# Optimization experiments

Measured on AMD Instinct MI355X. Metric: run time of the kernel, lower is better.

## Reference

```python
import jax, jax.numpy as jnp
import numpy as np

H = 768      # hidden_size
NH = 12      # num_heads
HD = H // NH # head_dim = 64


def setup_inputs() -> dict:
    key = jax.random.key(0)
    k1, k2, k3 = jax.random.split(key, 3)
    x = jax.random.normal(k1, (4, 2048, H), dtype=jnp.float32)
    # nn.Linear weights are [out, in]; we store transposed [in, out] for x @ W
    w_qkv = jax.random.normal(k2, (H, 3 * H), dtype=jnp.float32) * (1.0 / np.sqrt(H))
    w_out = jax.random.normal(k3, (H, H), dtype=jnp.float32) * (1.0 / np.sqrt(H))
    return {"x": x, "w_qkv": w_qkv, "w_out": w_out}


def reference(x, w_qkv, w_out):
    B, S, _ = x.shape
    qkv = (x @ w_qkv).reshape(B, S, 3, NH, HD)
    qkv = jnp.transpose(qkv, (2, 0, 3, 1, 4))  # [3, B, NH, S, HD]
    q, k, v = qkv[0], qkv[1], qkv[2]
    scale = 1.0 / np.sqrt(HD)
    scores = jnp.einsum('bhqd,bhkd->bhqk', q, k) * scale  # [B,NH,S,S]
    causal = jnp.tril(jnp.ones((S, S), dtype=bool))
    scores = jnp.where(causal, scores, jnp.finfo(scores.dtype).min)
    attn = jax.nn.softmax(scores, axis=-1)
    out = jnp.einsum('bhqk,bhkd->bhqd', attn, v)          # [B,NH,S,HD]
    out = jnp.transpose(out, (0, 2, 1, 3)).reshape(B, S, H)
    return out @ w_out
```

## Files before the change

kernel.cpp:

```cpp
#include <hip/hip_runtime.h>
#include <type_traits>

#define S_LEN 2048
#define HID   768
#define NHEAD 12
#define HDIM  64
#define BATCH 4

typedef __attribute__((ext_vector_type(4))) float float4v;
typedef __attribute__((ext_vector_type(8))) short short8;
typedef __attribute__((ext_vector_type(4))) short short4v;
typedef __attribute__((ext_vector_type(2))) int int2v;
typedef __attribute__((ext_vector_type(4))) int int4v;

__device__ __forceinline__ short f2b(float f) {
  unsigned u = __float_as_uint(f);
  u += 0x7fff + ((u >> 16) & 1);
  return (short)(u >> 16);
}

__device__ __forceinline__ unsigned pkbf(float a, float b) {
#if __has_builtin(__builtin_amdgcn_cvt_pk_bf16_f32)
  typedef __attribute__((ext_vector_type(2))) __bf16 bf2;
  bf2 r = __builtin_amdgcn_cvt_pk_bf16_f32(a, b);
  return *(unsigned*)&r;
#else
  return ((unsigned)(unsigned short)f2b(a)) |
         (((unsigned)(unsigned short)f2b(b)) << 16);
#endif
}

__device__ __forceinline__ float fexp2(float x) {
#if __has_builtin(__builtin_amdgcn_exp2f)
  return __builtin_amdgcn_exp2f(x);
#else
  return __expf(x * 0.69314718056f);
#endif
}

__device__ __forceinline__ void g2l16(const short* g, short* l) {
  __builtin_amdgcn_global_load_lds(
      (const __attribute__((address_space(1))) void*)g,
      (__attribute__((address_space(3))) void*)l, 16, 0, 0);
}

__global__ __launch_bounds__(256) void prepass(const float* __restrict__ x,
                                               const float* __restrict__ w_qkv,
                                               const float* __restrict__ w_out,
                                               short* __restrict__ xb,
                                               short* __restrict__ wqkvT,
                                               short* __restrict__ woutT) {
  __shared__ float tile[64][65];
  const int blk = blockIdx.x;
  if (blk < 3072) {
    int i = blk * 2048 + threadIdx.x * 8;
    float4v a = *(const float4v*)&x[i];
    float4v b = *(const float4v*)&x[i + 4];
    short8 o;
#pragma unroll
    for (int j = 0; j < 4; j++) { o[j] = f2b(a[j]); o[j + 4] = f2b(b[j]); }
    *(short8*)&xb[i] = o;
    return;
  }
  const float* W; short* WT; int N_, scaleN, idx;
  if (blk < 3504) { idx = blk - 3072; W = w_qkv; WT = wqkvT; N_ = 3 * HID; scaleN = HID; }
  else            { idx = blk - 3504; W = w_out; WT = woutT; N_ = HID;     scaleN = 0;  }
  const int nblk = N_ / 64;
  const int n0 = (idx % nblk) * 64, k0 = (idx / nblk) * 64;
  const int tx = threadIdx.x & 63, ty = threadIdx.x >> 6;
#pragma unroll
  for (int r = 0; r < 16; r++) {
    int row = r * 4 + ty;
    tile[row][tx] = W[(size_t)(k0 + row) * N_ + n0 + tx];
  }
  __syncthreads();
#pragma unroll
  for (int r = 0; r < 16; r++) {
    int row = r * 4 + ty;
    float sc = (n0 + row < scaleN) ? 0.18033688011f : 1.0f;
    WT[(size_t)(n0 + row) * HID + k0 + tx] = f2b(tile[tx][row] * sc);
  }
}

template <int OUT>
__global__ __launch_bounds__(256) void gemm_bt(const short* __restrict__ A,
                                               const short* __restrict__ Bt,
                                               float* __restrict__ Cf,
                                               short* __restrict__ Cq,
                                               short* __restrict__ vT,
                                               int M, int N, int K) {
  __shared__ __align__(16) short As[2][128 * 32];
  __shared__ __align__(16) short Bs[2][128 * 32];
  const int tid = threadIdx.x;
  const int w = tid >> 6, lane = tid & 63;
  const int quad = lane >> 4, lm = lane & 15;

  const int gx = gridDim.x;
  const int nwg = gx * gridDim.y;
  int flat = blockIdx.y * gx + blockIdx.x;
  if ((nwg & 7) == 0) flat = (flat & 7) * (nwg >> 3) + (flat >> 3);
  const int m0 = (flat / gx) * 128, n0 = (flat % gx) * 128;
  const int mo = (w & 1) * 64, no = (w >> 1) * 64;

  float4v acc[4][4];
#pragma unroll
  for (int i = 0; i < 4; i++)
#pragma unroll
    for (int j = 0; j < 4; j++) acc[i][j] = (float4v)0.0f;

  const int srow = w * 32 + (lane >> 2);
  const int scol = ((lane & 3) ^ ((lane >> 3) & 3)) * 8;
  const short* Ag = A + (size_t)(m0 + srow) * K + scol;
  const short* Bg = Bt + (size_t)(n0 + srow) * K + scol;

  const int qsw8 = (quad ^ ((lm >> 1) & 3)) * 8;

  for (int kb = 0; kb < K; kb += 64) {
#pragma unroll
    for (int s = 0; s < 2; s++) {
      short* Al = &As[s][(w * 32) * 32];
      short* Bl = &Bs[s][(w * 32) * 32];
      g2l16(Ag + kb + s * 32, Al);
      g2l16(Ag + kb + s * 32 + (size_t)16 * K, Al + 16 * 32);
      g2l16(Bg + kb + s * 32, Bl);
      g2l16(Bg + kb + s * 32 + (size_t)16 * K, Bl + 16 * 32);
    }
    __syncthreads();

#pragma unroll
    for (int s = 0; s < 2; s++) {
      short8 af[4], bf[4];
#pragma unroll
      for (int i = 0; i < 4; i++)
        af[i] = *(const short8*)&As[s][(mo + i * 16 + lm) * 32 + qsw8];
#pragma unroll
      for (int j = 0; j < 4; j++)
        bf[j] = *(const short8*)&Bs[s][(no + j * 16 + lm) * 32 + qsw8];
#pragma unroll
      for (int i = 0; i < 4; i++)
#pragma unroll
        for (int j = 0; j < 4; j++) {
          if constexpr (OUT == 2)
            acc[i][j] = __builtin_amdgcn_mfma_f32_16x16x32_bf16(bf[j], af[i], acc[i][j], 0, 0, 0);
          else
            acc[i][j] = __builtin_amdgcn_mfma_f32_16x16x32_bf16(af[i], bf[j], acc[i][j], 0, 0, 0);
        }
    }
    __syncthreads();
  }

  if constexpr (OUT == 0) {
#pragma unroll
    for (int i = 0; i < 4; i++)
#pragma unroll
      for (int j = 0; j < 4; j++)
#pragma unroll
        for (int r = 0; r < 4; r++)
          Cf[(size_t)(m0 + mo + i * 16 + quad * 4 + r) * N + n0 + no + j * 16 + lm] =
              acc[i][j][r];
  } else if constexpr (OUT == 1) {
#pragma unroll
    for (int i = 0; i < 4; i++)
#pragma unroll
      for (int j = 0; j < 4; j++)
#pragma unroll
        for (int r = 0; r < 4; r++)
          Cq[(size_t)(m0 + mo + i * 16 + quad * 4 + r) * (2 * HID) + n0 + no + j * 16 + lm] =
              f2b(acc[i][j][r]);
  } else {
    const int b = m0 >> 11;
#pragma unroll
    for (int i = 0; i < 4; i++) {
      const int sG = (m0 & 2047) + mo + i * 16 + lm;
#pragma unroll
      for (int j = 0; j < 4; j++) {
#pragma unroll
        for (int r = 0; r < 4; r++) {
          int col = n0 + no + j * 16 + quad * 4 + r;
          int h = col >> 6, d = col & 63;
          vT[((size_t)(b * NHEAD + h) * HDIM + d) * S_LEN + sG] = f2b(acc[i][j][r]);
        }
      }
    }
  }
}

__global__ __launch_bounds__(256) void attn_mfma(const short* __restrict__ qk,
                                                 const short* __restrict__ vT,
                                                 short* __restrict__ attnout) {
  __shared__ __align__(16) short Ks[2][64 * 64];
  __shared__ __align__(16) short Vt[2][64 * 64];

  const int tid = threadIdx.x;
  const int w = tid >> 6, lane = tid & 63;
  const int quad = lane >> 4, lm = lane & 15;
  const int bh = blockIdx.x;
  const int qt = 31 - blockIdx.y;
  const int b = bh / NHEAD, h = bh % NHEAD;

  short8 aq[2];
#pragma unroll
  for (int kb = 0; kb < 2; kb++)
    aq[kb] = *(const short8*)&qk[(size_t)(b * S_LEN + qt * 64 + w * 16 + lm) * (2 * HID) +
                                 h * HDIM + kb * 32 + quad * 8];

  const float4v z4 = (float4v)0.0f;
  short8 one8;
#pragma unroll
  for (int j = 0; j < 8; j++) one8[j] = (short)0x3F80;

  const size_t kbase = (size_t)(b * S_LEN) * (2 * HID) + HID + h * HDIM;
  const size_t vbase = (size_t)(b * NHEAD + h) * HDIM * S_LEN;
  const short* kptr[2];
  const short* vptr[2];
#pragma unroll
  for (int i = 0; i < 2; i++) {
    int c = (w * 2 + i) * 64 + lane;
    int row = c >> 3, slot = c & 7;
    int q8 = slot ^ (row & 7);
    int ra = row & 15, nt = row >> 4;
    int key = 8 * (ra >> 2) + 2 * (ra & 3) + (nt & 1) + 32 * (nt >> 1);
    kptr[i] = qk + kbase + (size_t)key * (2 * HID) + q8 * 8;
    vptr[i] = vT + vbase + (size_t)row * S_LEN + q8 * 8;
  }

#define ISSUE(BUF)                                                    \
  {                                                                   \
    _Pragma("unroll") for (int i = 0; i < 2; i++) {                   \
      g2l16(kptr[i], &Ks[BUF][(w * 2 + i) * 512]);                    \
      g2l16(vptr[i], &Vt[BUF][(w * 2 + i) * 512]);                    \
      kptr[i] += 64 * 2 * HID;                                        \
      vptr[i] += 64;                                                  \
    }                                                                 \
  }

  const int swx = (lm & 7) << 4;
  const int loff0 = (quad * 16) ^ swx;
  const int loff1 = (64 + quad * 16) ^ swx;
  const int rowK = lm << 7;
  const char* KsB = (const char*)&Ks[0][0];
  const char* VtB = (const char*)&Vt[0][0];

  float4v o_acc[4];
#pragma unroll
  for (int nt = 0; nt < 4; nt++) o_acc[nt] = (float4v)0.0f;
  float4v o1 = (float4v)0.0f;

  const int ktmax = qt + 1;
  int cur = 0;

  ISSUE(0);

  for (int kt = 0; kt < ktmax; kt++) {
    asm volatile("s_waitcnt vmcnt(0)" ::: "memory");
    __syncthreads();
    if (kt + 1 < ktmax) ISSUE(cur ^ 1);

    const int coff = cur << 13;
    const char* kB0 = KsB + coff + rowK + loff0;
    const char* kB1 = KsB + coff + rowK + loff1;
    const char* vB0 = VtB + coff + rowK + loff0;
    const char* vB1 = VtB + coff + rowK + loff1;

    float4v s_acc[4];
    __builtin_amdgcn_s_setprio(1);
#pragma unroll
    for (int nt = 0; nt < 4; nt++) {
      short8 bk = *(const short8*)(kB0 + nt * 2048);
      s_acc[nt] = __builtin_amdgcn_mfma_f32_16x16x32_bf16(bk, aq[0], z4, 0, 0, 0);
    }
#pragma unroll
    for (int nt = 0; nt < 4; nt++) {
      short8 bk = *(const short8*)(kB1 + nt * 2048);
      s_acc[nt] = __builtin_amdgcn_mfma_f32_16x16x32_bf16(bk, aq[1], s_acc[nt], 0, 0, 0);
    }
    __builtin_amdgcn_s_setprio(0);

    const bool diag = (kt == qt);
    float e[4][4];
#pragma unroll
    for (int nt = 0; nt < 4; nt++)
#pragma unroll
      for (int r = 0; r < 4; r++) {
        float v = fexp2(s_acc[nt][r]);
        if (diag && (8 * quad + 2 * r + (nt & 1) + 32 * (nt >> 1) > w * 16 + lm)) v = 0.0f;
        e[nt][r] = v;
      }

    int4v p0i = {(int)pkbf(e[0][0], e[1][0]), (int)pkbf(e[0][1], e[1][1]),
                 (int)pkbf(e[0][2], e[1][2]), (int)pkbf(e[0][3], e[1][3])};
    int4v p1i = {(int)pkbf(e[2][0], e[3][0]), (int)pkbf(e[2][1], e[3][1]),
                 (int)pkbf(e[2][2], e[3][2]), (int)pkbf(e[2][3], e[3][3])};
    union UU { int4v i; short8 s; };
    UU u0, u1;
    u0.i = p0i;
    u1.i = p1i;
    short8 ap0 = u0.s, ap1 = u1.s;

    __builtin_amdgcn_s_setprio(1);
    o1 = __builtin_amdgcn_mfma_f32_16x16x32_bf16(ap0, one8, o1, 0, 0, 0);
#pragma unroll
    for (int nt = 0; nt < 4; nt++) {
      short8 bv = *(const short8*)(vB0 + nt * 2048);
      o_acc[nt] = __builtin_amdgcn_mfma_f32_16x16x32_bf16(ap0, bv, o_acc[nt], 0, 0, 0);
    }
    o1 = __builtin_amdgcn_mfma_f32_16x16x32_bf16(ap1, one8, o1, 0, 0, 0);
#pragma unroll
    for (int nt = 0; nt < 4; nt++) {
      short8 bv = *(const short8*)(vB1 + nt * 2048);
      o_acc[nt] = __builtin_amdgcn_mfma_f32_16x16x32_bf16(ap1, bv, o_acc[nt], 0, 0, 0);
    }
    __builtin_amdgcn_s_setprio(0);

    cur ^= 1;
  }

#pragma unroll
  for (int r = 0; r < 4; r++) {
    float inv = 1.0f / o1[r];
    int rowg = b * S_LEN + qt * 64 + w * 16 + quad * 4 + r;
#pragma unroll
    for (int nt = 0; nt < 4; nt++)
      attnout[(size_t)rowg * HID + h * HDIM + nt * 16 + lm] =
          f2b(o_acc[nt][r] * inv);
  }
#undef ISSUE
}

extern "C" void kernel_launch(void* const* d_in, const int* in_sizes, int n_in,
                              void* d_out, int out_size, void* d_ws, size_t ws_size,
                              hipStream_t stream) {
  const float* x     = (const float*)d_in[0];
  const float* w_qkv = (const float*)d_in[1];
  const float* w_out = (const float*)d_in[2];
  float* out = (float*)d_out;

  const int M = BATCH * S_LEN;
  short* qk     = (short*)d_ws;
  short* attn   = qk + (size_t)M * 2 * HID;
  short* vT     = attn + (size_t)M * HID;
  short* xb     = vT + (size_t)M * HID;
  short* wqkvT  = xb + (size_t)M * HID;
  short* woutT  = wqkvT + (size_t)(3 * HID) * HID;

  prepass<<<3648, 256, 0, stream>>>(x, w_qkv, w_out, xb, wqkvT, woutT);

  gemm_bt<1><<<dim3(2 * HID / 128, M / 128), 256, 0, stream>>>(
      xb, wqkvT, nullptr, qk, nullptr, M, 2 * HID, HID);
  gemm_bt<2><<<dim3(HID / 128, M / 128), 256, 0, stream>>>(
      xb, wqkvT + (size_t)(2 * HID) * HID, nullptr, nullptr, vT, M, HID, HID);
  attn_mfma<<<dim3(BATCH * NHEAD, 32), 256, 0, stream>>>(qk, vT, attn);
  gemm_bt<0><<<dim3(HID / 128, M / 128), 256, 0, stream>>>(
      attn, woutT, out, nullptr, nullptr, M, HID, HID);
}
```

Measured before the change: 191.8 us.

## Software-pipeline attention loop: overlap QK^T of next tile with PV of previous

Restructures the attention inner loop so each iteration computes the QK^T MFMAs for tile kt, then the PV MFMAs for tile kt-1 using probabilities packed in the previous iteration, then the exp/pack for tile kt. This is meant to hide the exp/convert latency behind independent MFMA work. V staging grows to a triple buffer in LDS because V tiles are consumed one iteration later. The cost is more LDS and registers held across iterations, which may reduce occupancy.

```diff
diff --git a/kernel.cpp b/kernel.cpp
--- a/kernel.cpp
+++ b/kernel.cpp
@@ -12,6 +12,8 @@
 typedef __attribute__((ext_vector_type(4))) short short4v;
 typedef __attribute__((ext_vector_type(2))) int int2v;
 typedef __attribute__((ext_vector_type(4))) int int4v;
+
+union PU { int4v i; short8 s; };
 
 __device__ __forceinline__ short f2b(float f) {
   unsigned u = __float_as_uint(f);
@@ -189,7 +191,7 @@
                                                  const short* __restrict__ vT,
                                                  short* __restrict__ attnout) {
   __shared__ __align__(16) short Ks[2][64 * 64];
-  __shared__ __align__(16) short Vt[2][64 * 64];
+  __shared__ __align__(16) short Vt[3][64 * 64];
 
   const int tid = threadIdx.x;
   const int w = tid >> 6, lane = tid & 63;
@@ -224,14 +226,19 @@
     vptr[i] = vT + vbase + (size_t)row * S_LEN + q8 * 8;
   }
 
-#define ISSUE(BUF)                                                    \
-  {                                                                   \
-    _Pragma("unroll") for (int i = 0; i < 2; i++) {                   \
-      g2l16(kptr[i], &Ks[BUF][(w * 2 + i) * 512]);                    \
-      g2l16(vptr[i], &Vt[BUF][(w * 2 + i) * 512]);                    \
-      kptr[i] += 64 * 2 * HID;                                        \
-      vptr[i] += 64;                                                  \
-    }                                                                 \
+#define ISSUE_K(SLOT)                                                  \
+  {                                                                    \
+    _Pragma("unroll") for (int i = 0; i < 2; i++) {                    \
+      g2l16(kptr[i], &Ks[0][0] + (SLOT) * 4096 + (w * 2 + i) * 512);   \
+      kptr[i] += 64 * 2 * HID;                                         \
+    }                                                                  \
+  }
+#define ISSUE_V(SLOT)                                                  \
+  {                                                                    \
+    _Pragma("unroll") for (int i = 0; i < 2; i++) {                    \
+      g2l16(vptr[i], &Vt[0][0] + (SLOT) * 4096 + (w * 2 + i) * 512);   \
+      vptr[i] += 64;                                                   \
+    }                                                                  \
   }
 
   const int swx = (lm & 7) << 4;
@@ -246,73 +253,109 @@
   for (int nt = 0; nt < 4; nt++) o_acc[nt] = (float4v)0.0f;
   float4v o1 = (float4v)0.0f;
 
+#define QK_MFMA(KB0, KB1, SACC)                                                     \
+  {                                                                                 \
+    __builtin_amdgcn_s_setprio(1);                                                  \
+    _Pragma("unroll") for (int nt = 0; nt < 4; nt++) {                              \
+      short8 bk = *(const short8*)((KB0) + nt * 2048);                              \
+      SACC[nt] = __builtin_amdgcn_mfma_f32_16x16x32_bf16(bk, aq[0], z4, 0, 0, 0);   \
+    }                                                                               \
+    _Pragma("unroll") for (int nt = 0; nt < 4; nt++) {                              \
+      short8 bk = *(const short8*)((KB1) + nt * 2048);                              \
+      SACC[nt] =                                                                    \
+          __builtin_amdgcn_mfma_f32_16x16x32_bf16(bk, aq[1], SACC[nt], 0, 0, 0);    \
+    }                                                                               \
+    __builtin_amdgcn_s_setprio(0);                                                  \
+  }
+
+#define PV_MFMA(VB0, VB1, P0, P1)                                                   \
+  {                                                                                 \
+    __builtin_amdgcn_s_setprio(1);                                                  \
+    o1 = __builtin_amdgcn_mfma_f32_16x16x32_bf16(P0, one8, o1, 0, 0, 0);            \
+    _Pragma("unroll") for (int nt = 0; nt < 4; nt++) {                              \
+      short8 bv = *(const short8*)((VB0) + nt * 2048);                              \
+      o_acc[nt] =                                                                   \
+          __builtin_amdgcn_mfma_f32_16x16x32_bf16(P0, bv, o_acc[nt], 0, 0, 0);      \
+    }                                                                               \
+    o1 = __builtin_amdgcn_mfma_f32_16x16x32_bf16(P1, one8, o1, 0, 0, 0);            \
+    _Pragma("unroll") for (int nt = 0; nt < 4; nt++) {                              \
+      short8 bv = *(const short8*)((VB1) + nt * 2048);                              \
+      o_acc[nt] =                                                                   \
+          __builtin_amdgcn_mfma_f32_16x16x32_bf16(P1, bv, o_acc[nt], 0, 0, 0);      \
+    }                                                                               \
+    __builtin_amdgcn_s_setprio(0);                                                  \
+  }
+
+#define EXP_PACK(SACC, DIAG, P0, P1)                                                \
+  {                                                                                 \
+    float e[4][4];                                                                  \
+    _Pragma("unroll") for (int nt = 0; nt < 4; nt++)                                \
+      _Pragma("unroll") for (int r = 0; r < 4; r++) {                               \
+        float v = fexp2(SACC[nt][r]);                                               \
+        if ((DIAG) &&                                                               \
+            (8 * quad + 2 * r + (nt & 1) + 32 * (nt >> 1) > w * 16 + lm))           \
+          v = 0.0f;                                                                 \
+        e[nt][r] = v;                                                               \
+      }                                                                             \
+    int4v p0i = {(int)pkbf(e[0][0], e[1][0]), (int)pkbf(e[0][1], e[1][1]),          \
+                 (int)pkbf(e[0][2], e[1][2]), (int)pkbf(e[0][3], e[1][3])};         \
+    int4v p1i = {(int)pkbf(e[2][0], e[3][0]), (int)pkbf(e[2][1], e[3][1]),          \
+                 (int)pkbf(e[2][2], e[3][2]), (int)pkbf(e[2][3], e[3][3])};         \
+    PU u0, u1;                                                                      \
+    u0.i = p0i;                                                                     \
+    u1.i = p1i;                                                                     \
+    P0 = u0.s;                                                                      \
+    P1 = u1.s;                                                                      \
+  }
+
   const int ktmax = qt + 1;
-  int cur = 0;
-
-  ISSUE(0);
-
-  for (int kt = 0; kt < ktmax; kt++) {
+  short8 pp0, pp1;
+
+  ISSUE_K(0);
+  ISSUE_V(0);
+
+  asm volatile("s_waitcnt vmcnt(0)" ::: "memory");
+  __syncthreads();
+  if (ktmax > 1) { ISSUE_K(1); ISSUE_V(1); }
+  {
+    const char* kB0 = KsB + rowK + loff0;
+    const char* kB1 = KsB + rowK + loff1;
+    float4v s_acc[4];
+    QK_MFMA(kB0, kB1, s_acc);
+    const bool diag = (0 == qt);
+    EXP_PACK(s_acc, diag, pp0, pp1);
+  }
+
+  int krd = 1;
+  int vwr = 2;
+  int vrd = 0;
+
+  for (int kt = 1; kt < ktmax; kt++) {
     asm volatile("s_waitcnt vmcnt(0)" ::: "memory");
     __syncthreads();
-    if (kt + 1 < ktmax) ISSUE(cur ^ 1);
-
-    const int coff = cur << 13;
-    const char* kB0 = KsB + coff + rowK + loff0;
-    const char* kB1 = KsB + coff + rowK + loff1;
-    const char* vB0 = VtB + coff + rowK + loff0;
-    const char* vB1 = VtB + coff + rowK + loff1;
-
+    if (kt + 1 < ktmax) { ISSUE_K(krd ^ 1); ISSUE_V(vwr); }
+
+    const char* kB0 = KsB + (krd << 13) + rowK + loff0;
+    const char* kB1 = KsB + (krd << 13) + rowK + loff1;
     float4v s_acc[4];
-    __builtin_amdgcn_s_setprio(1);
-#pragma unroll
-    for (int nt = 0; nt < 4; nt++) {
-      short8 bk = *(const short8*)(kB0 + nt * 2048);
-      s_acc[nt] = __builtin_amdgcn_mfma_f32_16x16x32_bf16(bk, aq[0], z4, 0, 0, 0);
-    }
-#pragma unroll
-    for (int nt = 0; nt < 4; nt++) {
-      short8 bk = *(const short8*)(kB1 + nt * 2048);
-      s_acc[nt] = __builtin_amdgcn_mfma_f32_16x16x32_bf16(bk, aq[1], s_acc[nt], 0, 0, 0);
-    }
-    __builtin_amdgcn_s_setprio(0);
+    QK_MFMA(kB0, kB1, s_acc);
+
+    const char* vB0 = VtB + (vrd << 13) + rowK + loff0;
+    const char* vB1 = VtB + (vrd << 13) + rowK + loff1;
+    PV_MFMA(vB0, vB1, pp0, pp1);
 
     const bool diag = (kt == qt);
-    float e[4][4];
-#pragma unroll
-    for (int nt = 0; nt < 4; nt++)
-#pragma unroll
-      for (int r = 0; r < 4; r++) {
-        float v = fexp2(s_acc[nt][r]);
-        if (diag && (8 * quad + 2 * r + (nt & 1) + 32 * (nt >> 1) > w * 16 + lm)) v = 0.0f;
-        e[nt][r] = v;
-      }
-
-    int4v p0i = {(int)pkbf(e[0][0], e[1][0]), (int)pkbf(e[0][1], e[1][1]),
-                 (int)pkbf(e[0][2], e[1][2]), (int)pkbf(e[0][3], e[1][3])};
-    int4v p1i = {(int)pkbf(e[2][0], e[3][0]), (int)pkbf(e[2][1], e[3][1]),
-                 (int)pkbf(e[2][2], e[3][2]), (int)pkbf(e[2][3], e[3][3])};
-    union UU { int4v i; short8 s; };
-    UU u0, u1;
-    u0.i = p0i;
-    u1.i = p1i;
-    short8 ap0 = u0.s, ap1 = u1.s;
-
-    __builtin_amdgcn_s_setprio(1);
-    o1 = __builtin_amdgcn_mfma_f32_16x16x32_bf16(ap0, one8, o1, 0, 0, 0);
-#pragma unroll
-    for (int nt = 0; nt < 4; nt++) {
-      short8 bv = *(const short8*)(vB0 + nt * 2048);
-      o_acc[nt] = __builtin_amdgcn_mfma_f32_16x16x32_bf16(ap0, bv, o_acc[nt], 0, 0, 0);
-    }
-    o1 = __builtin_amdgcn_mfma_f32_16x16x32_bf16(ap1, one8, o1, 0, 0, 0);
-#pragma unroll
-    for (int nt = 0; nt < 4; nt++) {
-      short8 bv = *(const short8*)(vB1 + nt * 2048);
-      o_acc[nt] = __builtin_amdgcn_mfma_f32_16x16x32_bf16(ap1, bv, o_acc[nt], 0, 0, 0);
-    }
-    __builtin_amdgcn_s_setprio(0);
-
-    cur ^= 1;
+    EXP_PACK(s_acc, diag, pp0, pp1);
+
+    krd ^= 1;
+    vwr = (vwr == 2) ? 0 : vwr + 1;
+    vrd = (vrd == 2) ? 0 : vrd + 1;
+  }
+
+  {
+    const char* vB0 = VtB + (vrd << 13) + rowK + loff0;
+    const char* vB1 = VtB + (vrd << 13) + rowK + loff1;
+    PV_MFMA(vB0, vB1, pp0, pp1);
   }
 
 #pragma unroll
@@ -324,7 +367,11 @@
       attnout[(size_t)rowg * HID + h * HDIM + nt * 16 + lm] =
           f2b(o_acc[nt][r] * inv);
   }
-#undef ISSUE
+#undef ISSUE_K
+#undef ISSUE_V
+#undef QK_MFMA
+#undef PV_MFMA
+#undef EXP_PACK
 }
 
 extern "C" void kernel_launch(void* const* d_in, const int* in_sizes, int n_in,
```

Result: no change. 190.1 us (-0.9%).

## Process two adjacent query tiles per attention block to reuse K/V tiles

Applied to the files above, without the earlier changes.

Each attention workgroup now handles two consecutive 64-row query tiles (2a and 2a+1) instead of one. Every K/V tile staged into shared memory is used for both query tiles, roughly halving global K/V traffic and barrier count per query row. The grid shrinks from 32 to 16 blocks along y, which lowers parallelism to 768 blocks and raises register pressure from the doubled accumulators.

```diff
diff --git a/kernel.cpp b/kernel.cpp
--- a/kernel.cpp
+++ b/kernel.cpp
@@ -12,6 +12,8 @@
 typedef __attribute__((ext_vector_type(4))) short short4v;
 typedef __attribute__((ext_vector_type(2))) int int2v;
 typedef __attribute__((ext_vector_type(4))) int int4v;
+
+union PU { int4v i; short8 s; };
 
 __device__ __forceinline__ short f2b(float f) {
   unsigned u = __float_as_uint(f);
@@ -195,14 +197,18 @@
   const int w = tid >> 6, lane = tid & 63;
   const int quad = lane >> 4, lm = lane & 15;
   const int bh = blockIdx.x;
-  const int qt = 31 - blockIdx.y;
+  const int a = 15 - blockIdx.y;
+  const int qt0 = 2 * a, qt1 = 2 * a + 1;
   const int b = bh / NHEAD, h = bh % NHEAD;
 
-  short8 aq[2];
-#pragma unroll
-  for (int kb = 0; kb < 2; kb++)
-    aq[kb] = *(const short8*)&qk[(size_t)(b * S_LEN + qt * 64 + w * 16 + lm) * (2 * HID) +
-                                 h * HDIM + kb * 32 + quad * 8];
+  short8 aq0[2], aq1[2];
+#pragma unroll
+  for (int kb = 0; kb < 2; kb++) {
+    aq0[kb] = *(const short8*)&qk[(size_t)(b * S_LEN + qt0 * 64 + w * 16 + lm) * (2 * HID) +
+                                  h * HDIM + kb * 32 + quad * 8];
+    aq1[kb] = *(const short8*)&qk[(size_t)(b * S_LEN + qt1 * 64 + w * 16 + lm) * (2 * HID) +
+                                  h * HDIM + kb * 32 + quad * 8];
+  }
 
   const float4v z4 = (float4v)0.0f;
   short8 one8;
@@ -241,12 +247,63 @@
   const char* KsB = (const char*)&Ks[0][0];
   const char* VtB = (const char*)&Vt[0][0];
 
-  float4v o_acc[4];
-#pragma unroll
-  for (int nt = 0; nt < 4; nt++) o_acc[nt] = (float4v)0.0f;
-  float4v o1 = (float4v)0.0f;
-
-  const int ktmax = qt + 1;
+  float4v o_acc0[4], o_acc1[4];
+#pragma unroll
+  for (int nt = 0; nt < 4; nt++) { o_acc0[nt] = (float4v)0.0f; o_acc1[nt] = (float4v)0.0f; }
+  float4v o1v0 = (float4v)0.0f, o1v1 = (float4v)0.0f;
+
+#define QK_MFMA(AQ, KB0, KB1, SACC)                                                 \
+  {                                                                                 \
+    _Pragma("unroll") for (int nt = 0; nt < 4; nt++) {                              \
+      short8 bk = *(const short8*)((KB0) + nt * 2048);                              \
+      SACC[nt] = __builtin_amdgcn_mfma_f32_16x16x32_bf16(bk, AQ[0], z4, 0, 0, 0);   \
+    }                                                                               \
+    _Pragma("unroll") for (int nt = 0; nt < 4; nt++) {                              \
+      short8 bk = *(const short8*)((KB1) + nt * 2048);                              \
+      SACC[nt] =                                                                    \
+          __builtin_amdgcn_mfma_f32_16x16x32_bf16(bk, AQ[1], SACC[nt], 0, 0, 0);    \
+    }                                                                               \
+  }
+
+#define EXP_PACK(SACC, DIAG, P0, P1)                                                \
+  {                                                                                 \
+    float e[4][4];                                                                  \
+    _Pragma("unroll") for (int nt = 0; nt < 4; nt++)                                \
+      _Pragma("unroll") for (int r = 0; r < 4; r++) {                               \
+        float v = fexp2(SACC[nt][r]);                                               \
+        if ((DIAG) &&                                                               \
+            (8 * quad + 2 * r + (nt & 1) + 32 * (nt >> 1) > w * 16 + lm))           \
+          v = 0.0f;                                                                 \
+        e[nt][r] = v;                                                               \
+      }                                                                             \
+    int4v p0i = {(int)pkbf(e[0][0], e[1][0]), (int)pkbf(e[0][1], e[1][1]),          \
+                 (int)pkbf(e[0][2], e[1][2]), (int)pkbf(e[0][3], e[1][3])};         \
+    int4v p1i = {(int)pkbf(e[2][0], e[3][0]), (int)pkbf(e[2][1], e[3][1]),          \
+                 (int)pkbf(e[2][2], e[3][2]), (int)pkbf(e[2][3], e[3][3])};         \
+    PU u0, u1;                                                                      \
+    u0.i = p0i;                                                                     \
+    u1.i = p1i;                                                                     \
+    P0 = u0.s;                                                                      \
+    P1 = u1.s;                                                                      \
+  }
+
+#define PV_MFMA(OACC, O1, VB0, VB1, P0, P1)                                         \
+  {                                                                                 \
+    O1 = __builtin_amdgcn_mfma_f32_16x16x32_bf16(P0, one8, O1, 0, 0, 0);            \
+    _Pragma("unroll") for (int nt = 0; nt < 4; nt++) {                              \
+      short8 bv = *(const short8*)((VB0) + nt * 2048);                              \
+      OACC[nt] =                                                                    \
+          __builtin_amdgcn_mfma_f32_16x16x32_bf16(P0, bv, OACC[nt], 0, 0, 0);       \
+    }                                                                               \
+    O1 = __builtin_amdgcn_mfma_f32_16x16x32_bf16(P1, one8, O1, 0, 0, 0);            \
+    _Pragma("unroll") for (int nt = 0; nt < 4; nt++) {                              \
+      short8 bv = *(const short8*)((VB1) + nt * 2048);                              \
+      OACC[nt] =                                                                    \
+          __builtin_amdgcn_mfma_f32_16x16x32_bf16(P1, bv, OACC[nt], 0, 0, 0);       \
+    }                                                                               \
+  }
+
+  const int ktmax = qt1 + 1;
   int cur = 0;
 
   ISSUE(0);
@@ -262,69 +319,47 @@
     const char* vB0 = VtB + coff + rowK + loff0;
     const char* vB1 = VtB + coff + rowK + loff1;
 
-    float4v s_acc[4];
-    __builtin_amdgcn_s_setprio(1);
+    {
+      float4v s_acc[4];
+      __builtin_amdgcn_s_setprio(1);
+      QK_MFMA(aq1, kB0, kB1, s_acc);
+      __builtin_amdgcn_s_setprio(0);
+      short8 ap0, ap1;
+      EXP_PACK(s_acc, kt == qt1, ap0, ap1);
+      __builtin_amdgcn_s_setprio(1);
+      PV_MFMA(o_acc1, o1v1, vB0, vB1, ap0, ap1);
+      __builtin_amdgcn_s_setprio(0);
+    }
+    if (kt <= qt0) {
+      float4v s_acc[4];
+      __builtin_amdgcn_s_setprio(1);
+      QK_MFMA(aq0, kB0, kB1, s_acc);
+      __builtin_amdgcn_s_setprio(0);
+      short8 ap0, ap1;
+      EXP_PACK(s_acc, kt == qt0, ap0, ap1);
+      __builtin_amdgcn_s_setprio(1);
+      PV_MFMA(o_acc0, o1v0, vB0, vB1, ap0, ap1);
+      __builtin_amdgcn_s_setprio(0);
+    }
+    cur ^= 1;
+  }
+
+#pragma unroll
+  for (int r = 0; r < 4; r++) {
+    float inv1 = 1.0f / o1v1[r];
+    float inv0 = 1.0f / o1v0[r];
+    int rowg1 = b * S_LEN + qt1 * 64 + w * 16 + quad * 4 + r;
+    int rowg0 = b * S_LEN + qt0 * 64 + w * 16 + quad * 4 + r;
 #pragma unroll
     for (int nt = 0; nt < 4; nt++) {
-      short8 bk = *(const short8*)(kB0 + nt * 2048);
-      s_acc[nt] = __builtin_amdgcn_mfma_f32_16x16x32_bf16(bk, aq[0], z4, 0, 0, 0);
-    }
-#pragma unroll
-    for (int nt = 0; nt < 4; nt++) {
-      short8 bk = *(const short8*)(kB1 + nt * 2048);
-      s_acc[nt] = __builtin_amdgcn_mfma_f32_16x16x32_bf16(bk, aq[1], s_acc[nt], 0, 0, 0);
-    }
-    __builtin_amdgcn_s_setprio(0);
-
-    const bool diag = (kt == qt);
-    float e[4][4];
-#pragma unroll
-    for (int nt = 0; nt < 4; nt++)
-#pragma unroll
-      for (int r = 0; r < 4; r++) {
-        float v = fexp2(s_acc[nt][r]);
-        if (diag && (8 * quad + 2 * r + (nt & 1) + 32 * (nt >> 1) > w * 16 + lm)) v = 0.0f;
-        e[nt][r] = v;
-      }
-
-    int4v p0i = {(int)pkbf(e[0][0], e[1][0]), (int)pkbf(e[0][1], e[1][1]),
-                 (int)pkbf(e[0][2], e[1][2]), (int)pkbf(e[0][3], e[1][3])};
-    int4v p1i = {(int)pkbf(e[2][0], e[3][0]), (int)pkbf(e[2][1], e[3][1]),
-                 (int)pkbf(e[2][2], e[3][2]), (int)pkbf(e[2][3], e[3][3])};
-    union UU { int4v i; short8 s; };
-    UU u0, u1;
-    u0.i = p0i;
-    u1.i = p1i;
-    short8 ap0 = u0.s, ap1 = u1.s;
-
-    __builtin_amdgcn_s_setprio(1);
-    o1 = __builtin_amdgcn_mfma_f32_16x16x32_bf16(ap0, one8, o1, 0, 0, 0);
-#pragma unroll
-    for (int nt = 0; nt < 4; nt++) {
-      short8 bv = *(const short8*)(vB0 + nt * 2048);
-      o_acc[nt] = __builtin_amdgcn_mfma_f32_16x16x32_bf16(ap0, bv, o_acc[nt], 0, 0, 0);
-    }
-    o1 = __builtin_amdgcn_mfma_f32_16x16x32_bf16(ap1, one8, o1, 0, 0, 0);
-#pragma unroll
-    for (int nt = 0; nt < 4; nt++) {
-      short8 bv = *(const short8*)(vB1 + nt * 2048);
-      o_acc[nt] = __builtin_amdgcn_mfma_f32_16x16x32_bf16(ap1, bv, o_acc[nt], 0, 0, 0);
-    }
-    __builtin_amdgcn_s_setprio(0);
-
-    cur ^= 1;
-  }
-
-#pragma unroll
-  for (int r = 0; r < 4; r++) {
-    float inv = 1.0f / o1[r];
-    int rowg = b * S_LEN + qt * 64 + w * 16 + quad * 4 + r;
-#pragma unroll
-    for (int nt = 0; nt < 4; nt++)
-      attnout[(size_t)rowg * HID + h * HDIM + nt * 16 + lm] =
-          f2b(o_acc[nt][r] * inv);
+      attnout[(size_t)rowg1 * HID + h * HDIM + nt * 16 + lm] = f2b(o_acc1[nt][r] * inv1);
+      attnout[(size_t)rowg0 * HID + h * HDIM + nt * 16 + lm] = f2b(o_acc0[nt][r] * inv0);
+    }
   }
 #undef ISSUE
+#undef QK_MFMA
+#undef EXP_PACK
+#undef PV_MFMA
 }
 
 extern "C" void kernel_launch(void* const* d_in, const int* in_sizes, int n_in,
@@ -349,7 +384,7 @@
       xb, wqkvT, nullptr, qk, nullptr, M, 2 * HID, HID);
   gemm_bt<2><<<dim3(HID / 128, M / 128), 256, 0, stream>>>(
       xb, wqkvT + (size_t)(2 * HID) * HID, nullptr, nullptr, vT, M, HID, HID);
-  attn_mfma<<<dim3(BATCH * NHEAD, 32), 256, 0, stream>>>(qk, vT, attn);
+  attn_mfma<<<dim3(BATCH * NHEAD, 16), 256, 0, stream>>>(qk, vT, attn);
   gemm_bt<0><<<dim3(HID / 128, M / 128), 256, 0, stream>>>(
       attn, woutT, out, nullptr, nullptr, M, HID, HID);
 }
```

Result: slower. 200.0 us (+4.3%).
